# Performance work log

Measured on AMD Instinct MI355X. Metric: run time of the kernel, lower is better.

Reference implementation:

```python
import jax, jax.numpy as jnp
import numpy as np
from math import factorial, sqrt

MUL = 128
BATCH = 16384
IRREPS_IN1 = [(MUL, 0, 1), (MUL, 1, -1), (MUL, 2, 1)]   # (mul, l, parity)
IRREPS_IN2 = [(1, 0, 1), (1, 1, -1), (1, 2, 1), (1, 3, -1)]
TARGET = {(0, 1), (1, -1), (2, 1), (3, -1)}               # allowed output (l, parity)


def _su2_cg(j1, m1, j2, m2, j3, m3):
    """Complex Clebsch-Gordan coefficient <j1 m1 j2 m2 | j3 m3> (Racah formula)."""
    if m1 + m2 != m3:
        return 0.0
    f = lambda n: float(factorial(n))
    pref = sqrt((2 * j3 + 1) * f(j1 + j2 - j3) * f(j1 - j2 + j3) * f(-j1 + j2 + j3) / f(j1 + j2 + j3 + 1))
    pref *= sqrt(f(j1 + m1) * f(j1 - m1) * f(j2 + m2) * f(j2 - m2) * f(j3 + m3) * f(j3 - m3))
    s = 0.0
    lo = max(0, j2 - j3 - m1, j1 - j3 + m2)
    hi = min(j1 + j2 - j3, j1 - m1, j2 + m2)
    for k in range(lo, hi + 1):
        s += (-1.0) ** k / (f(k) * f(j1 + j2 - j3 - k) * f(j1 - m1 - k) * f(j2 + m2 - k) * f(j3 - j2 + m1 + k) * f(j3 - j1 - m2 + k))
    return pref * s


def _q(l):
    """Change of basis real SH <- complex SH (e3nn convention, phased)."""
    q = np.zeros((2 * l + 1, 2 * l + 1), dtype=np.complex128)
    for m in range(-l, 0):
        q[l + m, l + abs(m)] = 1.0 / np.sqrt(2)
        q[l + m, l - abs(m)] = -1j / np.sqrt(2)
    q[l, l] = 1.0
    for m in range(1, l + 1):
        q[l + m, l + abs(m)] = (-1) ** m / np.sqrt(2)
        q[l + m, l - abs(m)] = 1j * (-1) ** m / np.sqrt(2)
    return (-1j) ** l * q


def _real_cg(l1, l2, l3):
    """Real-basis CG tensor [2l1+1, 2l2+1, 2l3+1], unit Frobenius norm."""
    Cc = np.zeros((2 * l1 + 1, 2 * l2 + 1, 2 * l3 + 1), dtype=np.complex128)
    for a, m1 in enumerate(range(-l1, l1 + 1)):
        for b, m2 in enumerate(range(-l2, l2 + 1)):
            for c, m3 in enumerate(range(-l3, l3 + 1)):
                Cc[a, b, c] = _su2_cg(l1, m1, l2, m2, l3, m3)
    C = np.einsum('abc,ia,jb,kc->ijk', Cc, np.conj(_q(l1)), np.conj(_q(l2)), _q(l3))
    re, im = np.real(C), np.imag(C)
    C = re if np.linalg.norm(re) >= np.linalg.norm(im) else im  # result is real up to a global phase
    return (C / np.linalg.norm(C)).astype(np.float32)


# enumerate channelwise ('uvu', mul2 == 1) paths allowed by CG selection rules + TARGET filter
PATHS = []
for i, (m1, l1, p1) in enumerate(IRREPS_IN1):
    for j, (m2, l2, p2) in enumerate(IRREPS_IN2):
        for l3 in range(abs(l1 - l2), l1 + l2 + 1):
            if (l3, p1 * p2) in TARGET:
                PATHS.append((i, j, l3))
ORDER = sorted(range(len(PATHS)), key=lambda k: PATHS[k][2])  # stable sort by output l
CG = {(IRREPS_IN1[i][1], IRREPS_IN2[j][1], l3): _real_cg(IRREPS_IN1[i][1], IRREPS_IN2[j][1], l3)
      for (i, j, l3) in PATHS}

OFF1 = np.cumsum([0] + [m * (2 * l + 1) for m, l, _ in IRREPS_IN1])
OFF2 = np.cumsum([0] + [m * (2 * l + 1) for m, l, _ in IRREPS_IN2])
DIM1, DIM2 = int(OFF1[-1]), int(OFF2[-1])          # 1152, 16
WEIGHT_NUMEL = MUL * len(PATHS)                     # 17 * 128 = 2176
DIM_OUT = sum(MUL * (2 * PATHS[k][2] + 1) for k in ORDER)  # 9088


def setup_inputs() -> dict:
    key = jax.random.key(0)
    k1, k2, k3 = jax.random.split(key, 3)
    return {
        'x1': jax.random.normal(k1, (BATCH, DIM1), dtype=jnp.float32),
        'x2': jax.random.normal(k2, (BATCH, DIM2), dtype=jnp.float32),
        'weights': jax.random.normal(k3, (BATCH, WEIGHT_NUMEL), dtype=jnp.float32),
    }


def reference(x1, x2, weights):
    B = x1.shape[0]
    # split mul_ir inputs into per-irrep segments
    x1s = [x1[:, int(OFF1[i]):int(OFF1[i + 1])].reshape(B, m, 2 * l + 1)
           for i, (m, l, _) in enumerate(IRREPS_IN1)]
    x2s = [x2[:, int(OFF2[j]):int(OFF2[j + 1])] for j in range(len(IRREPS_IN2))]  # mul2 == 1
    outs = []
    for k in ORDER:
        i, j, l3 = PATHS[k]
        l1, l2 = IRREPS_IN1[i][1], IRREPS_IN2[j][1]
        C = jnp.asarray(CG[(l1, l2, l3)])                  # [2l1+1, 2l2+1, 2l3+1]
        w = weights[:, k * MUL:(k + 1) * MUL]              # [B, mul] per-edge per-channel weights
        alpha = sqrt((2 * l3 + 1) / MUL)                   # component/element path normalization
        y = jnp.einsum('ijk,bui,bj->buk', C, x1s[i], x2s[j])  # [B, mul, 2l3+1]
        outs.append((alpha * w[:, :, None] * y).reshape(B, MUL * (2 * l3 + 1)))
    return jnp.concatenate(outs, axis=1)  # mul_ir layout, one slot per path, sorted by output l
```

## Files before the change

kernel.cpp:

```cpp
#include <hip/hip_runtime.h>


#define NPATH 17

__device__ const int d_PL1[NPATH]  = {0,0,0,0, 1,1,1,1,1,1, 2,2,2,2,2,2,2};
__device__ const int d_PL2[NPATH]  = {0,1,2,3, 0,1,1,2,2,3, 0,1,1,2,2,3,3};
__device__ const int d_PL3[NPATH]  = {0,1,2,3, 1,0,2,1,3,2, 2,1,3,0,2,1,3};
__device__ const int d_CGOFF[NPATH] = {0,1,10,35,84,93,102,147,192,297,402,427,472,577,602,727,832};
__device__ const int d_X2OFF[NPATH] = {0,1,4,9, 0,1,1,4,4,9, 0,1,1,4,4,9,9};
__device__ const int d_KOFF[NPATH]  = {0,4,8,16,24,36,40,56,68,92,108,136,152,188,196,224,240};
__device__ const int d_KN[NPATH]    = {1,3,5,7, 9,3,15,9,21,15, 25,15,35,5,25,15,35};

__device__ float g_cg[1077];


__device__ double dfactd(int n){ double r=1.0; for(int i=2;i<=n;++i) r *= (double)i; return r; }

__device__ double su2cg(int j1,int m1,int j2,int m2,int j3,int m3){
  if (m1+m2 != m3) return 0.0;
  double pref = sqrt((double)(2*j3+1)*dfactd(j1+j2-j3)*dfactd(j1-j2+j3)*dfactd(-j1+j2+j3)/dfactd(j1+j2+j3+1));
  pref *= sqrt(dfactd(j1+m1)*dfactd(j1-m1)*dfactd(j2+m2)*dfactd(j2-m2)*dfactd(j3+m3)*dfactd(j3-m3));
  int lo = 0;
  if (j2-j3-m1 > lo) lo = j2-j3-m1;
  if (j1-j3+m2 > lo) lo = j1-j3+m2;
  int hi = j1+j2-j3;
  if (j1-m1 < hi) hi = j1-m1;
  if (j2+m2 < hi) hi = j2+m2;
  double s = 0.0;
  for (int k=lo;k<=hi;++k){
    double d = dfactd(k)*dfactd(j1+j2-j3-k)*dfactd(j1-m1-k)*dfactd(j2+m2-k)
             * dfactd(j3-j2+m1+k)*dfactd(j3-j1-m2+k);
    s += ((k&1) ? -1.0 : 1.0)/d;
  }
  return pref*s;
}

struct Cplx { double re, im; };

__device__ int qrow(int l, int r, int* cols, Cplx* vals){
  const double is2 = 0.70710678118654752440;
  int mp = r - l;
  int n;
  double vr[2], vi[2];
  if (mp < 0)      { cols[0]=l-mp; vr[0]=is2;  vi[0]=0.0;  cols[1]=l+mp; vr[1]=0.0; vi[1]=-is2; n=2; }
  else if (mp==0)  { cols[0]=l;    vr[0]=1.0;  vi[0]=0.0;  n=1; }
  else { double sg = (mp&1)? -1.0 : 1.0;
         cols[0]=l+mp; vr[0]=sg*is2; vi[0]=0.0;
         cols[1]=l-mp; vr[1]=0.0;    vi[1]=sg*is2; n=2; }
  int ph = l & 3;
  for (int t=0;t<n;++t){
    double re=vr[t], im=vi[t], nr, ni;
    if      (ph==0){ nr=re;  ni=im;  }
    else if (ph==1){ nr=im;  ni=-re; }
    else if (ph==2){ nr=-re; ni=-im; }
    else           { nr=-im; ni=re;  }
    vals[t].re=nr; vals[t].im=ni;
  }
  return n;
}

__global__ void tp_cg_setup(){
  const int p = blockIdx.x;
  const int l1=d_PL1[p], l2=d_PL2[p], l3=d_PL3[p];
  const int N2=2*l2+1, N3=2*l3+1;
  const int n = (2*l1+1)*N2*N3;
  __shared__ double sre[245], sim[245];
  for (int e=threadIdx.x; e<n; e+=blockDim.x){
    int k = e % N3, rem = e / N3;
    int j = rem % N2, i = rem / N2;
    int ca[2], cb[2], cc[2];
    Cplx va[2], vb[2], vc[2];
    int na=qrow(l1,i,ca,va), nb=qrow(l2,j,cb,vb), nc=qrow(l3,k,cc,vc);
    double ar=0.0, ai=0.0;
    for (int a=0;a<na;++a) for (int b=0;b<nb;++b){
      double r1=va[a].re, i1=-va[a].im;
      double r2=vb[b].re, i2=-vb[b].im;
      double r12 = r1*r2 - i1*i2;
      double i12 = r1*i2 + i1*r2;
      for (int c=0;c<nc;++c){
        double cg = su2cg(l1, ca[a]-l1, l2, cb[b]-l2, l3, cc[c]-l3);
        if (cg != 0.0){
          double r3=vc[c].re, i3=vc[c].im;
          ar += cg*(r12*r3 - i12*i3);
          ai += cg*(r12*i3 + i12*r3);
        }
      }
    }
    sre[e]=ar; sim[e]=ai;
  }
  __syncthreads();
  __shared__ double s_scale;
  __shared__ int s_usere;
  if (threadIdx.x==0){
    double nr=0.0, ni=0.0;
    for (int e=0;e<n;++e){ nr += sre[e]*sre[e]; ni += sim[e]*sim[e]; }
    int ur = (nr >= ni) ? 1 : 0;
    s_usere = ur;
    s_scale = 1.0/sqrt(ur ? nr : ni);
  }
  __syncthreads();
  const int off = d_CGOFF[p];
  for (int e=threadIdx.x; e<n; e+=blockDim.x)
    g_cg[off+e] = (float)((s_usere ? sre[e] : sim[e]) * s_scale);
}


template<int L1, int L3>
__device__ __forceinline__ void path_out(const float* __restrict__ Kp,
                                         const float* __restrict__ xv,
                                         float wa, float* __restrict__ op){
  constexpr int N1 = 2*L1+1, N3 = 2*L3+1;
  float y[N3];
#pragma unroll
  for (int k=0;k<N3;++k) y[k] = 0.0f;
#pragma unroll
  for (int i=0;i<N1;++i){
    const float a = xv[i];
#pragma unroll
    for (int k=0;k<N3;++k) y[k] = fmaf(Kp[i*N3+k], a, y[k]);
  }
#pragma unroll
  for (int k=0;k<N3;++k) op[k] = wa*y[k];
}

__global__ __launch_bounds__(256) void tp_main(const float* __restrict__ x1,
                                               const float* __restrict__ x2,
                                               const float* __restrict__ wts,
                                               float* __restrict__ out){
  __shared__ float sK[2][276];
  const int tid = threadIdx.x;
  const int bb  = tid >> 7;
  const int u   = tid & 127;
  const long long b = (long long)blockIdx.x*2 + bb;

  {
    const float* __restrict__ x2b = x2 + b*16;
    for (int e=u; e<243; e+=128){
      int p=0, rem=e;
      while (rem >= d_KN[p]) { rem -= d_KN[p]; ++p; }
      const int N3 = 2*d_PL3[p]+1;
      const int N2 = 2*d_PL2[p]+1;
      const int i  = rem / N3;
      const float* __restrict__ C  = g_cg + d_CGOFF[p] + (i*N2)*N3 + (rem % N3);
      const float* __restrict__ xx = x2b + d_X2OFF[p];
      float acc = 0.f;
      for (int j=0;j<N2;++j) acc = fmaf(C[j*N3], xx[j], acc);
      sK[bb][d_KOFF[p] + rem] = acc;
    }
  }
  __syncthreads();

  const float* __restrict__ x1b = x1 + b*1152;
  float xv[9];
  xv[0] = x1b[u];
#pragma unroll
  for (int t=0;t<3;++t) xv[1+t] = x1b[128 + 3*u + t];
#pragma unroll
  for (int t=0;t<5;++t) xv[4+t] = x1b[512 + 5*u + t];
  const float* __restrict__ wb  = wts + b*2176 + u;
  float* __restrict__ outb      = out + b*9088;
  const float* __restrict__ K   = sK[bb];

  const float A0=0.08838834764831845f, A1=0.15309310892394863f,
              A2=0.19764235376052372f, A3=0.23385358667337133f;

  path_out<0,0>(K+0,   xv+0, wb[0*128]*A0,  outb + 0    + u);
  path_out<0,1>(K+4,   xv+0, wb[1*128]*A1,  outb + 384  + u*3);
  path_out<0,2>(K+8,   xv+0, wb[2*128]*A2,  outb + 2304 + u*5);
  path_out<0,3>(K+16,  xv+0, wb[3*128]*A3,  outb + 5504 + u*7);
  path_out<1,1>(K+24,  xv+1, wb[4*128]*A1,  outb + 768  + u*3);
  path_out<1,0>(K+36,  xv+1, wb[5*128]*A0,  outb + 128  + u);
  path_out<1,2>(K+40,  xv+1, wb[6*128]*A2,  outb + 2944 + u*5);
  path_out<1,1>(K+56,  xv+1, wb[7*128]*A1,  outb + 1152 + u*3);
  path_out<1,3>(K+68,  xv+1, wb[8*128]*A3,  outb + 6400 + u*7);
  path_out<1,2>(K+92,  xv+1, wb[9*128]*A2,  outb + 3584 + u*5);
  path_out<2,2>(K+108, xv+4, wb[10*128]*A2, outb + 4224 + u*5);
  path_out<2,1>(K+136, xv+4, wb[11*128]*A1, outb + 1536 + u*3);
  path_out<2,3>(K+152, xv+4, wb[12*128]*A3, outb + 7296 + u*7);
  path_out<2,0>(K+188, xv+4, wb[13*128]*A0, outb + 256  + u);
  path_out<2,2>(K+196, xv+4, wb[14*128]*A2, outb + 4864 + u*5);
  path_out<2,1>(K+224, xv+4, wb[15*128]*A1, outb + 1920 + u*3);
  path_out<2,3>(K+240, xv+4, wb[16*128]*A3, outb + 8192 + u*7);
}


extern "C" void kernel_launch(void* const* d_in, const int* in_sizes, int n_in,
                              void* d_out, int out_size, void* d_ws, size_t ws_size,
                              hipStream_t stream) {
  const float* x1 = (const float*)d_in[0];
  const float* x2 = (const float*)d_in[1];
  const float* w  = (const float*)d_in[2];
  float* out = (float*)d_out;
  (void)d_ws; (void)ws_size; (void)in_sizes; (void)n_in; (void)out_size;

  tp_cg_setup<<<dim3(NPATH), dim3(256), 0, stream>>>();
  tp_main<<<dim3(16384/2), dim3(256), 0, stream>>>(x1, x2, w, out);
}
```

Measured before the change: 208.0 us.

## Stage outputs in shared memory for coalesced float4 stores, one batch per block

```diff
diff --git a/kernel.cpp b/kernel.cpp
--- a/kernel.cpp
+++ b/kernel.cpp
@@ -127,60 +127,72 @@
                                                const float* __restrict__ x2,
                                                const float* __restrict__ wts,
                                                float* __restrict__ out){
-  __shared__ float sK[2][276];
+  __shared__ float sK[276];
+  __shared__ __align__(16) float sOut[9088];
   const int tid = threadIdx.x;
-  const int bb  = tid >> 7;
+  const int t   = tid >> 7;
   const int u   = tid & 127;
-  const long long b = (long long)blockIdx.x*2 + bb;
+  const long long b = blockIdx.x;
+
+  if (tid < 243){
+    const float* __restrict__ x2b = x2 + b*16;
+    int p=0, rem=tid;
+    while (rem >= d_KN[p]) { rem -= d_KN[p]; ++p; }
+    const int N3 = 2*d_PL3[p]+1;
+    const int N2 = 2*d_PL2[p]+1;
+    const int i  = rem / N3;
+    const float* __restrict__ C  = g_cg + d_CGOFF[p] + (i*N2)*N3 + (rem % N3);
+    const float* __restrict__ xx = x2b + d_X2OFF[p];
+    float acc = 0.f;
+    for (int j=0;j<N2;++j) acc = fmaf(C[j*N3], xx[j], acc);
+    sK[d_KOFF[p] + rem] = acc;
+  }
+  __syncthreads();
 
   {
-    const float* __restrict__ x2b = x2 + b*16;
-    for (int e=u; e<243; e+=128){
-      int p=0, rem=e;
-      while (rem >= d_KN[p]) { rem -= d_KN[p]; ++p; }
-      const int N3 = 2*d_PL3[p]+1;
-      const int N2 = 2*d_PL2[p]+1;
-      const int i  = rem / N3;
-      const float* __restrict__ C  = g_cg + d_CGOFF[p] + (i*N2)*N3 + (rem % N3);
-      const float* __restrict__ xx = x2b + d_X2OFF[p];
-      float acc = 0.f;
-      for (int j=0;j<N2;++j) acc = fmaf(C[j*N3], xx[j], acc);
-      sK[bb][d_KOFF[p] + rem] = acc;
+    const float* __restrict__ x1b = x1 + b*1152;
+    const float* __restrict__ wb  = wts + b*2176 + u;
+    const float* __restrict__ K   = sK;
+
+    const float A0=0.08838834764831845f, A1=0.15309310892394863f,
+                A2=0.19764235376052372f, A3=0.23385358667337133f;
+
+    if (t == 0){
+      float xv[4];
+      xv[0] = x1b[u];
+#pragma unroll
+      for (int q=0;q<3;++q) xv[1+q] = x1b[128 + 3*u + q];
+      path_out<0,0>(K+0,   xv+0, wb[0*128]*A0,  sOut + 0    + u);
+      path_out<0,1>(K+4,   xv+0, wb[1*128]*A1,  sOut + 384  + u*3);
+      path_out<0,2>(K+8,   xv+0, wb[2*128]*A2,  sOut + 2304 + u*5);
+      path_out<0,3>(K+16,  xv+0, wb[3*128]*A3,  sOut + 5504 + u*7);
+      path_out<1,1>(K+24,  xv+1, wb[4*128]*A1,  sOut + 768  + u*3);
+      path_out<1,0>(K+36,  xv+1, wb[5*128]*A0,  sOut + 128  + u);
+      path_out<1,2>(K+40,  xv+1, wb[6*128]*A2,  sOut + 2944 + u*5);
+      path_out<1,1>(K+56,  xv+1, wb[7*128]*A1,  sOut + 1152 + u*3);
+      path_out<1,3>(K+68,  xv+1, wb[8*128]*A3,  sOut + 6400 + u*7);
+      path_out<1,2>(K+92,  xv+1, wb[9*128]*A2,  sOut + 3584 + u*5);
+    } else {
+      float xv[5];
+#pragma unroll
+      for (int q=0;q<5;++q) xv[q] = x1b[512 + 5*u + q];
+      path_out<2,2>(K+108, xv, wb[10*128]*A2, sOut + 4224 + u*5);
+      path_out<2,1>(K+136, xv, wb[11*128]*A1, sOut + 1536 + u*3);
+      path_out<2,3>(K+152, xv, wb[12*128]*A3, sOut + 7296 + u*7);
+      path_out<2,0>(K+188, xv, wb[13*128]*A0, sOut + 256  + u);
+      path_out<2,2>(K+196, xv, wb[14*128]*A2, sOut + 4864 + u*5);
+      path_out<2,1>(K+224, xv, wb[15*128]*A1, sOut + 1920 + u*3);
+      path_out<2,3>(K+240, xv, wb[16*128]*A3, sOut + 8192 + u*7);
     }
   }
   __syncthreads();
 
-  const float* __restrict__ x1b = x1 + b*1152;
-  float xv[9];
-  xv[0] = x1b[u];
-#pragma unroll
-  for (int t=0;t<3;++t) xv[1+t] = x1b[128 + 3*u + t];
-#pragma unroll
-  for (int t=0;t<5;++t) xv[4+t] = x1b[512 + 5*u + t];
-  const float* __restrict__ wb  = wts + b*2176 + u;
-  float* __restrict__ outb      = out + b*9088;
-  const float* __restrict__ K   = sK[bb];
-
-  const float A0=0.08838834764831845f, A1=0.15309310892394863f,
-              A2=0.19764235376052372f, A3=0.23385358667337133f;
-
-  path_out<0,0>(K+0,   xv+0, wb[0*128]*A0,  outb + 0    + u);
-  path_out<0,1>(K+4,   xv+0, wb[1*128]*A1,  outb + 384  + u*3);
-  path_out<0,2>(K+8,   xv+0, wb[2*128]*A2,  outb + 2304 + u*5);
-  path_out<0,3>(K+16,  xv+0, wb[3*128]*A3,  outb + 5504 + u*7);
-  path_out<1,1>(K+24,  xv+1, wb[4*128]*A1,  outb + 768  + u*3);
-  path_out<1,0>(K+36,  xv+1, wb[5*128]*A0,  outb + 128  + u);
-  path_out<1,2>(K+40,  xv+1, wb[6*128]*A2,  outb + 2944 + u*5);
-  path_out<1,1>(K+56,  xv+1, wb[7*128]*A1,  outb + 1152 + u*3);
-  path_out<1,3>(K+68,  xv+1, wb[8*128]*A3,  outb + 6400 + u*7);
-  path_out<1,2>(K+92,  xv+1, wb[9*128]*A2,  outb + 3584 + u*5);
-  path_out<2,2>(K+108, xv+4, wb[10*128]*A2, outb + 4224 + u*5);
-  path_out<2,1>(K+136, xv+4, wb[11*128]*A1, outb + 1536 + u*3);
-  path_out<2,3>(K+152, xv+4, wb[12*128]*A3, outb + 7296 + u*7);
-  path_out<2,0>(K+188, xv+4, wb[13*128]*A0, outb + 256  + u);
-  path_out<2,2>(K+196, xv+4, wb[14*128]*A2, outb + 4864 + u*5);
-  path_out<2,1>(K+224, xv+4, wb[15*128]*A1, outb + 1920 + u*3);
-  path_out<2,3>(K+240, xv+4, wb[16*128]*A3, outb + 8192 + u*7);
+  {
+    float4* __restrict__ dst = (float4*)(out + b*9088);
+    const float4* __restrict__ src = (const float4*)sOut;
+    for (int idx = tid; idx < 2272; idx += 256)
+      dst[idx] = src[idx];
+  }
 }
 
 
@@ -194,5 +206,5 @@
   (void)d_ws; (void)ws_size; (void)in_sizes; (void)n_in; (void)out_size;
 
   tp_cg_setup<<<dim3(NPATH), dim3(256), 0, stream>>>();
-  tp_main<<<dim3(16384/2), dim3(256), 0, stream>>>(x1, x2, w, out);
-}
+  tp_main<<<dim3(16384), dim3(256), 0, stream>>>(x1, x2, w, out);
+}
```

After: 188.4 us. 9.4% less time.
